# Kernel optimization log

Measured on AMD Instinct MI355X. Metric: run time of the kernel, lower is better.

The kernel has to match this reference:

```python
import jax, jax.numpy as jnp
import numpy as np

N_HEAD = 16


def setup_inputs() -> dict:
    key = jax.random.key(0)
    ks = jax.random.split(key, 5)
    B, T, C = 4, 2048, 1024
    s = 1.0 / np.sqrt(C)
    x = jax.random.normal(ks[0], (B, T, C), dtype=jnp.float32)
    wq = jax.random.normal(ks[1], (C, C), dtype=jnp.float32) * s
    wk = jax.random.normal(ks[2], (C, C), dtype=jnp.float32) * s
    wv = jax.random.normal(ks[3], (C, C), dtype=jnp.float32) * s
    wo = jax.random.normal(ks[4], (C, C), dtype=jnp.float32) * s
    return {"x": x, "wq": wq, "wk": wk, "wv": wv, "wo": wo}


def _attn(x, wq, wk, wv, wo):
    B, T, C = x.shape
    H = N_HEAD
    D = C // H
    scale = 1.0 / np.sqrt(D)
    # nn.Linear(x) = x @ W.T; weights stored as [out, in]
    q = (x @ wq.T).reshape(B, T, H, D).transpose(0, 2, 1, 3)  # [B,H,T,D]
    k = (x @ wk.T).reshape(B, T, H, D).transpose(0, 2, 1, 3)
    v = (x @ wv.T).reshape(B, T, H, D).transpose(0, 2, 1, 3)
    scores = jnp.einsum("bhtd,bhsd->bhts", q, k) * scale  # [B,H,T,T]
    mask = jnp.triu(jnp.full((T, T), -jnp.inf, dtype=scores.dtype), k=1)
    attn = jax.nn.softmax(scores + mask, axis=-1)
    out = jnp.einsum("bhts,bhsd->bhtd", attn, v)  # [B,H,T,D]
    out = out.transpose(0, 2, 1, 3).reshape(B, T, C)
    return out @ wo.T


def reference(x, wq, wk, wv, wo):
    return _attn(x, wq, wk, wv, wo)
```

## Files before the change

### kernel.cpp

```cpp
#include <hip/hip_runtime.h>

typedef __bf16 bf16x8 __attribute__((ext_vector_type(8)));
typedef float f32x4 __attribute__((ext_vector_type(4)));
typedef unsigned short ushortx8 __attribute__((ext_vector_type(8)));
typedef unsigned short ushortx4 __attribute__((ext_vector_type(4)));

#if __has_builtin(__builtin_amdgcn_exp2f)
#define EXP2F(x) __builtin_amdgcn_exp2f(x)
#else
#define EXP2F(x) exp2f(x)
#endif
#if __has_builtin(__builtin_amdgcn_rcpf)
#define RCPF(x) __builtin_amdgcn_rcpf(x)
#else
#define RCPF(x) (1.0f / (x))
#endif

__device__ __forceinline__ unsigned short f2bf(float f) {
    unsigned int u = __builtin_bit_cast(unsigned int, f);
    u += 0x7fffu + ((u >> 16) & 1u);
    return (unsigned short)(u >> 16);
}

__device__ __forceinline__ bf16x8 ld_frag(const unsigned short* p) {
    return __builtin_bit_cast(bf16x8, *(const ushortx8*)p);
}

__device__ __forceinline__ unsigned int pack_bf2(float lo, float hi) {
#if __has_builtin(__builtin_amdgcn_cvt_pk_bf16_f32)
    typedef __bf16 bf16x2 __attribute__((ext_vector_type(2)));
    bf16x2 v = __builtin_amdgcn_cvt_pk_bf16_f32(lo, hi);
    return __builtin_bit_cast(unsigned int, v);
#else
    unsigned int ulo = __builtin_bit_cast(unsigned int, lo) + 0x8000u;
    unsigned int uhi = __builtin_bit_cast(unsigned int, hi) + 0x8000u;
    return __builtin_amdgcn_perm(uhi, ulo, 0x07060302u);
#endif
}

__device__ __forceinline__ void async_cp16(const unsigned short* g, unsigned short* l) {
    __builtin_amdgcn_global_load_lds(
        (const __attribute__((address_space(1))) unsigned int*)g,
        (__attribute__((address_space(3))) unsigned int*)(unsigned long)(unsigned long long)(uintptr_t)
            reinterpret_cast<uintptr_t>(l),
        16, 0, 0);
}

__global__ void cvt_kernel(const float* __restrict__ src, unsigned short* __restrict__ dst, int n4) {
    int i = blockIdx.x * blockDim.x + threadIdx.x;
    if (i < n4) {
        float4 f = ((const float4*)src)[i];
        ushortx4 u = { f2bf(f.x), f2bf(f.y), f2bf(f.z), f2bf(f.w) };
        ((ushortx4*)dst)[i] = u;
    }
}

__global__ void cvt4_kernel(const float* __restrict__ s0, const float* __restrict__ s1,
                            const float* __restrict__ s2, const float* __restrict__ s3,
                            unsigned short* __restrict__ dst) {
    const float* src = (blockIdx.y == 0) ? s0 : (blockIdx.y == 1) ? s1 : (blockIdx.y == 2) ? s2 : s3;
    unsigned short* d = dst + (size_t)blockIdx.y * (1024 * 1024);
    int i = blockIdx.x * blockDim.x + threadIdx.x;
    float4 f = ((const float4*)src)[i];
    ushortx4 u = { f2bf(f.x), f2bf(f.y), f2bf(f.z), f2bf(f.w) };
    ((ushortx4*)d)[i] = u;
}

__global__ __launch_bounds__(256, 3) void qkv_gemm(
    const unsigned short* __restrict__ xb,
    const unsigned short* __restrict__ wqb,
    const unsigned short* __restrict__ wkb,
    const unsigned short* __restrict__ wvb,
    unsigned short* __restrict__ q_ws,
    unsigned short* __restrict__ k_ws,
    unsigned short* __restrict__ v_ws)
{
    __shared__ __align__(16) unsigned short A_lds[128 * 32];
    __shared__ __align__(16) unsigned short B_lds[128 * 32];

    const int tid = threadIdx.x;
    const int wv = tid >> 6;
    const int lane = tid & 63;
    const int quad = lane >> 4;
    const int l15 = lane & 15;
    const int wm = wv >> 1;
    const int wn = wv & 1;

    const int m0 = blockIdx.x * 128;
    const int mat = blockIdx.y >> 3;
    const int n0 = (blockIdx.y & 7) * 128;
    const unsigned short* wb = (mat == 0) ? wqb : (mat == 1 ? wkb : wvb);

    const int srow = lane >> 2;
    const int scol = (lane & 3) * 8;
    const unsigned short* ag0 = xb + (size_t)(m0 + wv * 32 + srow) * 1024 + scol;
    const unsigned short* ag1 = ag0 + 16 * 1024;
    const unsigned short* bg0 = wb + (size_t)(n0 + wv * 32 + srow) * 1024 + scol;
    const unsigned short* bg1 = bg0 + 16 * 1024;
    unsigned short* la0 = A_lds + (wv * 32) * 32;
    unsigned short* la1 = A_lds + (wv * 32 + 16) * 32;
    unsigned short* lb0 = B_lds + (wv * 32) * 32;
    unsigned short* lb1 = B_lds + (wv * 32 + 16) * 32;

    f32x4 acc[4][4] = {};

    for (int kt = 0; kt < 1024; kt += 32) {
        __syncthreads();
        async_cp16(ag0 + kt, la0);
        async_cp16(ag1 + kt, la1);
        async_cp16(bg0 + kt, lb0);
        async_cp16(bg1 + kt, lb1);
        __builtin_amdgcn_s_waitcnt(0x0F70);
        __syncthreads();

        bf16x8 af[4], bf[4];
#pragma unroll
        for (int i = 0; i < 4; ++i)
            af[i] = ld_frag(A_lds + (wm * 64 + i * 16 + l15) * 32 + quad * 8);
#pragma unroll
        for (int i = 0; i < 4; ++i)
            bf[i] = ld_frag(B_lds + (wn * 64 + i * 16 + l15) * 32 + quad * 8);
#pragma unroll
        for (int i = 0; i < 4; ++i)
#pragma unroll
            for (int j = 0; j < 4; ++j)
                acc[i][j] = __builtin_amdgcn_mfma_f32_16x16x32_bf16(af[i], bf[j], acc[i][j], 0, 0, 0);
    }

    const float qscale = 0.125f * 1.4426950408889634f;
    const int mbase = m0 + wm * 64;
    const int nbase = n0 + wn * 64;
#pragma unroll
    for (int i = 0; i < 4; ++i) {
        const int mrow = mbase + i * 16 + quad * 4;
        const int b = mrow >> 11;
        const int trow = mrow & 2047;
#pragma unroll
        for (int j = 0; j < 4; ++j) {
            const int nloc = nbase + j * 16 + l15;
            const int h = nloc >> 6, d = nloc & 63;
            if (mat == 2) {
                ushortx4 pk = { f2bf(acc[i][j][0]), f2bf(acc[i][j][1]),
                                f2bf(acc[i][j][2]), f2bf(acc[i][j][3]) };
                *(ushortx4*)&v_ws[(((size_t)(b * 16 + h)) * 64 + d) * 2048 + trow] = pk;
            } else {
                unsigned short* dst = (mat == 0) ? q_ws : k_ws;
                float sc = (mat == 0) ? qscale : 1.0f;
                size_t base = (((size_t)(b * 16 + h)) * 2048 + trow) * 64 + d;
                dst[base]       = f2bf(acc[i][j][0] * sc);
                dst[base + 64]  = f2bf(acc[i][j][1] * sc);
                dst[base + 128] = f2bf(acc[i][j][2] * sc);
                dst[base + 192] = f2bf(acc[i][j][3] * sc);
            }
        }
    }
}

__global__ __launch_bounds__(256, 2) void attn_kernel(
    const unsigned short* __restrict__ q_ws,
    const unsigned short* __restrict__ k_ws,
    const unsigned short* __restrict__ v_ws,
    unsigned short* __restrict__ o_ws)
{
    __shared__ __align__(16) unsigned short K_lds[128][72];
    __shared__ __align__(16) unsigned short Vt_lds[64][136];
    __shared__ __align__(16) unsigned short P_lds[128][136];

    const int tid = threadIdx.x;
    const int wvid = tid >> 6, lane = tid & 63, quad = lane >> 4, l15 = lane & 15;
    const int bh = blockIdx.x;
    const int b = bh >> 4, h = bh & 15;
    const int bt = 15 - (int)blockIdx.y;
    const int t0 = bt * 128;

    const unsigned short* qb = q_ws + (size_t)bh * 2048 * 64;
    const unsigned short* kb = k_ws + (size_t)bh * 2048 * 64;
    const unsigned short* vb = v_ws + (size_t)bh * 64 * 2048;

    ushortx8 ones_u = { 0x3F80, 0x3F80, 0x3F80, 0x3F80, 0x3F80, 0x3F80, 0x3F80, 0x3F80 };
    const bf16x8 ones = __builtin_bit_cast(bf16x8, ones_u);

    bf16x8 bq[2][2];
#pragma unroll
    for (int it = 0; it < 2; ++it)
#pragma unroll
        for (int kk = 0; kk < 2; ++kk)
            bq[it][kk] = ld_frag(qb + (size_t)(t0 + wvid * 32 + it * 16 + l15) * 64 + kk * 32 + quad * 8);

    f32x4 acc_o[2][4] = {};
    f32x4 l_acc[2] = {};

    const int kr = tid >> 1, kc = (tid & 1) * 32;
    const int vr = tid >> 2, vc = (tid & 3) * 32;

    for (int j = 0; j <= bt; ++j) {
        const int s0 = j * 128;
        ushortx8 kvr[4], vvr[4];
#pragma unroll
        for (int u = 0; u < 4; ++u)
            kvr[u] = *(const ushortx8*)(kb + (size_t)(s0 + kr) * 64 + kc + u * 8);
#pragma unroll
        for (int u = 0; u < 4; ++u)
            vvr[u] = *(const ushortx8*)(vb + (size_t)vr * 2048 + s0 + vc + u * 8);
        __syncthreads();
#pragma unroll
        for (int u = 0; u < 4; ++u) *(ushortx8*)&K_lds[kr][kc + u * 8] = kvr[u];
#pragma unroll
        for (int u = 0; u < 4; ++u) *(ushortx8*)&Vt_lds[vr][vc + u * 8] = vvr[u];
        __syncthreads();

        f32x4 sacc[2][8] = {};
#pragma unroll
        for (int is = 0; is < 8; ++is) {
            bf16x8 k0 = ld_frag(&K_lds[is * 16 + l15][quad * 8]);
            bf16x8 k1 = ld_frag(&K_lds[is * 16 + l15][32 + quad * 8]);
            sacc[0][is] = __builtin_amdgcn_mfma_f32_16x16x32_bf16(k0, bq[0][0], sacc[0][is], 0, 0, 0);
            sacc[0][is] = __builtin_amdgcn_mfma_f32_16x16x32_bf16(k1, bq[0][1], sacc[0][is], 0, 0, 0);
            sacc[1][is] = __builtin_amdgcn_mfma_f32_16x16x32_bf16(k0, bq[1][0], sacc[1][is], 0, 0, 0);
            sacc[1][is] = __builtin_amdgcn_mfma_f32_16x16x32_bf16(k1, bq[1][1], sacc[1][is], 0, 0, 0);
        }

        if (j == bt) {
#pragma unroll
            for (int it = 0; it < 2; ++it) {
                const int tl = wvid * 32 + it * 16 + l15;
#pragma unroll
                for (int is = 0; is < 8; ++is)
#pragma unroll
                    for (int r = 0; r < 4; ++r) {
                        const int sl = is * 16 + quad * 4 + r;
                        if (sl > tl) sacc[it][is][r] = -1.0e30f;
                    }
            }
        }

#pragma unroll
        for (int it = 0; it < 2; ++it) {
            const int row = wvid * 32 + it * 16 + l15;
#pragma unroll
            for (int is = 0; is < 8; ++is) {
                float p0 = EXP2F(sacc[it][is][0]);
                float p1 = EXP2F(sacc[it][is][1]);
                float p2 = EXP2F(sacc[it][is][2]);
                float p3 = EXP2F(sacc[it][is][3]);
                uint2 pk = { pack_bf2(p0, p1), pack_bf2(p2, p3) };
                *(uint2*)&P_lds[row][is * 16 + quad * 4] = pk;
            }
        }

        __threadfence_block();

#pragma unroll
        for (int kk = 0; kk < 4; ++kk) {
            bf16x8 p0 = ld_frag(&P_lds[wvid * 32 + l15][kk * 32 + quad * 8]);
            bf16x8 p1 = ld_frag(&P_lds[wvid * 32 + 16 + l15][kk * 32 + quad * 8]);
            l_acc[0] = __builtin_amdgcn_mfma_f32_16x16x32_bf16(p0, ones, l_acc[0], 0, 0, 0);
            l_acc[1] = __builtin_amdgcn_mfma_f32_16x16x32_bf16(p1, ones, l_acc[1], 0, 0, 0);
#pragma unroll
            for (int id = 0; id < 4; ++id) {
                bf16x8 bv = ld_frag(&Vt_lds[id * 16 + l15][kk * 32 + quad * 8]);
                acc_o[0][id] = __builtin_amdgcn_mfma_f32_16x16x32_bf16(p0, bv, acc_o[0][id], 0, 0, 0);
                acc_o[1][id] = __builtin_amdgcn_mfma_f32_16x16x32_bf16(p1, bv, acc_o[1][id], 0, 0, 0);
            }
        }
    }

#pragma unroll
    for (int it = 0; it < 2; ++it) {
        f32x4 rinv;
#pragma unroll
        for (int r = 0; r < 4; ++r) rinv[r] = RCPF(l_acc[it][r]);
#pragma unroll
        for (int id = 0; id < 4; ++id)
#pragma unroll
            for (int r = 0; r < 4; ++r) {
                int tg = t0 + wvid * 32 + it * 16 + quad * 4 + r;
                int c = h * 64 + id * 16 + l15;
                o_ws[(size_t)(b * 2048 + tg) * 1024 + c] = f2bf(acc_o[it][id][r] * rinv[r]);
            }
    }
}

__global__ __launch_bounds__(256, 3) void out_gemm(
    const unsigned short* __restrict__ ob,
    const unsigned short* __restrict__ wob,
    float* __restrict__ out)
{
    __shared__ __align__(16) unsigned short A_lds[128 * 32];
    __shared__ __align__(16) unsigned short B_lds[128 * 32];

    const int tid = threadIdx.x;
    const int wv = tid >> 6;
    const int lane = tid & 63;
    const int quad = lane >> 4;
    const int l15 = lane & 15;
    const int wm = wv >> 1;
    const int wn = wv & 1;

    const int m0 = blockIdx.x * 128;
    const int n0 = blockIdx.y * 128;

    const int srow = lane >> 2;
    const int scol = (lane & 3) * 8;
    const unsigned short* ag0 = ob + (size_t)(m0 + wv * 32 + srow) * 1024 + scol;
    const unsigned short* ag1 = ag0 + 16 * 1024;
    const unsigned short* bg0 = wob + (size_t)(n0 + wv * 32 + srow) * 1024 + scol;
    const unsigned short* bg1 = bg0 + 16 * 1024;
    unsigned short* la0 = A_lds + (wv * 32) * 32;
    unsigned short* la1 = A_lds + (wv * 32 + 16) * 32;
    unsigned short* lb0 = B_lds + (wv * 32) * 32;
    unsigned short* lb1 = B_lds + (wv * 32 + 16) * 32;

    f32x4 acc[4][4] = {};

    for (int kt = 0; kt < 1024; kt += 32) {
        __syncthreads();
        async_cp16(ag0 + kt, la0);
        async_cp16(ag1 + kt, la1);
        async_cp16(bg0 + kt, lb0);
        async_cp16(bg1 + kt, lb1);
        __builtin_amdgcn_s_waitcnt(0x0F70);
        __syncthreads();

        bf16x8 af[4], bf[4];
#pragma unroll
        for (int i = 0; i < 4; ++i)
            af[i] = ld_frag(A_lds + (wm * 64 + i * 16 + l15) * 32 + quad * 8);
#pragma unroll
        for (int i = 0; i < 4; ++i)
            bf[i] = ld_frag(B_lds + (wn * 64 + i * 16 + l15) * 32 + quad * 8);
#pragma unroll
        for (int i = 0; i < 4; ++i)
#pragma unroll
            for (int j = 0; j < 4; ++j)
                acc[i][j] = __builtin_amdgcn_mfma_f32_16x16x32_bf16(af[i], bf[j], acc[i][j], 0, 0, 0);
    }

    const int mbase = m0 + wm * 64;
    const int nbase = n0 + wn * 64;
#pragma unroll
    for (int i = 0; i < 4; ++i) {
        const int mrow = mbase + i * 16 + quad * 4;
#pragma unroll
        for (int j = 0; j < 4; ++j) {
            const int ncol = nbase + j * 16 + l15;
            float* dst = out + (size_t)mrow * 1024 + ncol;
            dst[0]        = acc[i][j][0];
            dst[1024]     = acc[i][j][1];
            dst[2048]     = acc[i][j][2];
            dst[3072]     = acc[i][j][3];
        }
    }
}

extern "C" void kernel_launch(void* const* d_in, const int* in_sizes, int n_in,
                              void* d_out, int out_size, void* d_ws, size_t ws_size,
                              hipStream_t stream) {
    const float* x  = (const float*)d_in[0];
    const float* wq = (const float*)d_in[1];
    const float* wk = (const float*)d_in[2];
    const float* wv = (const float*)d_in[3];
    const float* wo = (const float*)d_in[4];
    float* out = (float*)d_out;

    unsigned short* ws = (unsigned short*)d_ws;
    unsigned short* xb   = ws;
    unsigned short* wqb  = xb  + (size_t)8192 * 1024;
    unsigned short* wkb  = wqb + (size_t)1024 * 1024;
    unsigned short* wvb  = wkb + (size_t)1024 * 1024;
    unsigned short* wob  = wvb + (size_t)1024 * 1024;
    unsigned short* q_ws = wob + (size_t)1024 * 1024;
    unsigned short* k_ws = q_ws + (size_t)8192 * 1024;
    unsigned short* v_ws = k_ws + (size_t)8192 * 1024;
    unsigned short* o_ws = v_ws + (size_t)8192 * 1024;

    int n4 = (8192 * 1024) / 4;
    cvt_kernel<<<(n4 + 255) / 256, 256, 0, stream>>>(x, xb, n4);
    cvt4_kernel<<<dim3(1024, 4), 256, 0, stream>>>(wq, wk, wv, wo, wqb);

    qkv_gemm<<<dim3(64, 24), 256, 0, stream>>>(xb, wqb, wkb, wvb, q_ws, k_ws, v_ws);
    attn_kernel<<<dim3(64, 16), 256, 0, stream>>>(q_ws, k_ws, v_ws, o_ws);
    out_gemm<<<dim3(64, 8), 256, 0, stream>>>(o_ws, wob, out);
}
```

Baseline: 238.4 us.

## Prefetch next K/V tile into registers, raise MFMA priority, merge conversion kernels

The attention loop now loads the next K/V tile from global memory into registers right after the current tile is stored to LDS, so global latency overlaps the current tile's MFMA and softmax work. MFMA sections are wrapped in s_setprio hints, and the block-level fence before reading P is replaced with an explicit lgkmcnt wait plus a scheduling barrier. The two fp32-to-bf16 conversion kernels are merged into one launch to remove a kernel boundary. The cost is higher register pressure from the live prefetch registers, which could reduce occupancy.

```diff
diff --git a/kernel.cpp b/kernel.cpp
--- a/kernel.cpp
+++ b/kernel.cpp
@@ -46,24 +46,26 @@
         16, 0, 0);
 }
 
-__global__ void cvt_kernel(const float* __restrict__ src, unsigned short* __restrict__ dst, int n4) {
+__global__ void cvt_all_kernel(const float* __restrict__ x,
+                               const float* __restrict__ wq, const float* __restrict__ wk,
+                               const float* __restrict__ wv, const float* __restrict__ wo,
+                               unsigned short* __restrict__ xb,
+                               unsigned short* __restrict__ wqb) {
+    const int NX4 = (8192 * 1024) / 4;
     int i = blockIdx.x * blockDim.x + threadIdx.x;
-    if (i < n4) {
-        float4 f = ((const float4*)src)[i];
+    if (i < NX4) {
+        float4 f = ((const float4*)x)[i];
         ushortx4 u = { f2bf(f.x), f2bf(f.y), f2bf(f.z), f2bf(f.w) };
-        ((ushortx4*)dst)[i] = u;
-    }
-}
-
-__global__ void cvt4_kernel(const float* __restrict__ s0, const float* __restrict__ s1,
-                            const float* __restrict__ s2, const float* __restrict__ s3,
-                            unsigned short* __restrict__ dst) {
-    const float* src = (blockIdx.y == 0) ? s0 : (blockIdx.y == 1) ? s1 : (blockIdx.y == 2) ? s2 : s3;
-    unsigned short* d = dst + (size_t)blockIdx.y * (1024 * 1024);
-    int i = blockIdx.x * blockDim.x + threadIdx.x;
-    float4 f = ((const float4*)src)[i];
-    ushortx4 u = { f2bf(f.x), f2bf(f.y), f2bf(f.z), f2bf(f.w) };
-    ((ushortx4*)d)[i] = u;
+        ((ushortx4*)xb)[i] = u;
+    } else {
+        int k = i - NX4;
+        int w = k >> 18;
+        int r = k & 0x3FFFF;
+        const float* src = (w == 0) ? wq : (w == 1) ? wk : (w == 2) ? wv : wo;
+        float4 f = ((const float4*)src)[r];
+        ushortx4 u = { f2bf(f.x), f2bf(f.y), f2bf(f.z), f2bf(f.w) };
+        ((ushortx4*)wqb)[k] = u;
+    }
 }
 
 __global__ __launch_bounds__(256, 3) void qkv_gemm(
@@ -193,15 +195,15 @@
     const int kr = tid >> 1, kc = (tid & 1) * 32;
     const int vr = tid >> 2, vc = (tid & 3) * 32;
 
+    ushortx8 kvr[4], vvr[4];
+#pragma unroll
+    for (int u = 0; u < 4; ++u)
+        kvr[u] = *(const ushortx8*)(kb + (size_t)kr * 64 + kc + u * 8);
+#pragma unroll
+    for (int u = 0; u < 4; ++u)
+        vvr[u] = *(const ushortx8*)(vb + (size_t)vr * 2048 + vc + u * 8);
+
     for (int j = 0; j <= bt; ++j) {
-        const int s0 = j * 128;
-        ushortx8 kvr[4], vvr[4];
-#pragma unroll
-        for (int u = 0; u < 4; ++u)
-            kvr[u] = *(const ushortx8*)(kb + (size_t)(s0 + kr) * 64 + kc + u * 8);
-#pragma unroll
-        for (int u = 0; u < 4; ++u)
-            vvr[u] = *(const ushortx8*)(vb + (size_t)vr * 2048 + s0 + vc + u * 8);
         __syncthreads();
 #pragma unroll
         for (int u = 0; u < 4; ++u) *(ushortx8*)&K_lds[kr][kc + u * 8] = kvr[u];
@@ -209,7 +211,18 @@
         for (int u = 0; u < 4; ++u) *(ushortx8*)&Vt_lds[vr][vc + u * 8] = vvr[u];
         __syncthreads();
 
+        if (j < bt) {
+            const int s1 = (j + 1) * 128;
+#pragma unroll
+            for (int u = 0; u < 4; ++u)
+                kvr[u] = *(const ushortx8*)(kb + (size_t)(s1 + kr) * 64 + kc + u * 8);
+#pragma unroll
+            for (int u = 0; u < 4; ++u)
+                vvr[u] = *(const ushortx8*)(vb + (size_t)vr * 2048 + s1 + vc + u * 8);
+        }
+
         f32x4 sacc[2][8] = {};
+        __builtin_amdgcn_s_setprio(1);
 #pragma unroll
         for (int is = 0; is < 8; ++is) {
             bf16x8 k0 = ld_frag(&K_lds[is * 16 + l15][quad * 8]);
@@ -219,6 +232,7 @@
             sacc[1][is] = __builtin_amdgcn_mfma_f32_16x16x32_bf16(k0, bq[1][0], sacc[1][is], 0, 0, 0);
             sacc[1][is] = __builtin_amdgcn_mfma_f32_16x16x32_bf16(k1, bq[1][1], sacc[1][is], 0, 0, 0);
         }
+        __builtin_amdgcn_s_setprio(0);
 
         if (j == bt) {
 #pragma unroll
@@ -248,12 +262,14 @@
             }
         }
 
-        __threadfence_block();
+        asm volatile("s_waitcnt lgkmcnt(0)" ::: "memory");
+        __builtin_amdgcn_sched_barrier(0);
 
 #pragma unroll
         for (int kk = 0; kk < 4; ++kk) {
             bf16x8 p0 = ld_frag(&P_lds[wvid * 32 + l15][kk * 32 + quad * 8]);
             bf16x8 p1 = ld_frag(&P_lds[wvid * 32 + 16 + l15][kk * 32 + quad * 8]);
+            __builtin_amdgcn_s_setprio(1);
             l_acc[0] = __builtin_amdgcn_mfma_f32_16x16x32_bf16(p0, ones, l_acc[0], 0, 0, 0);
             l_acc[1] = __builtin_amdgcn_mfma_f32_16x16x32_bf16(p1, ones, l_acc[1], 0, 0, 0);
 #pragma unroll
@@ -262,6 +278,7 @@
                 acc_o[0][id] = __builtin_amdgcn_mfma_f32_16x16x32_bf16(p0, bv, acc_o[0][id], 0, 0, 0);
                 acc_o[1][id] = __builtin_amdgcn_mfma_f32_16x16x32_bf16(p1, bv, acc_o[1][id], 0, 0, 0);
             }
+            __builtin_amdgcn_s_setprio(0);
         }
     }
 
@@ -374,9 +391,8 @@
     unsigned short* v_ws = k_ws + (size_t)8192 * 1024;
     unsigned short* o_ws = v_ws + (size_t)8192 * 1024;
 
-    int n4 = (8192 * 1024) / 4;
-    cvt_kernel<<<(n4 + 255) / 256, 256, 0, stream>>>(x, xb, n4);
-    cvt4_kernel<<<dim3(1024, 4), 256, 0, stream>>>(wq, wk, wv, wo, wqb);
+    int total4 = (8192 * 1024 + 4 * 1024 * 1024) / 4;
+    cvt_all_kernel<<<(total4 + 255) / 256, 256, 0, stream>>>(x, wq, wk, wv, wo, xb, wqb);
 
     qkv_gemm<<<dim3(64, 24), 256, 0, stream>>>(xb, wqb, wkb, wvb, q_ws, k_ws, v_ws);
     attn_kernel<<<dim3(64, 16), 256, 0, stream>>>(q_ws, k_ws, v_ws, o_ws);
```

Measured after the change: 238.1 us. About the same (-0.1%).
